# Kernel optimization log

Hardware: AMD Instinct MI355X
Metric: run time of the kernel (lower is better)

## Reference

```python
import jax, jax.numpy as jnp
import numpy as np

N = 50000        # nodes
R = 51           # enriched relations (25 fwd + 25 inverse + self-loop)
F_IN = 32        # feat_size
E = 32           # embed_size
C = 16           # num_classes
B = 30           # num_bases
NNZ = 2_000_000  # nonzeros in vertical adjacency


def _xavier(key, shape):
    # mimics nn.init.xavier_uniform_ with gain for relu (sqrt(2))
    fan_in, fan_out = shape[-2], shape[-1]
    a = np.sqrt(2.0) * np.sqrt(6.0 / (fan_in + fan_out))
    return jax.random.uniform(key, shape, jnp.float32, -a, a)


def setup_inputs() -> dict:
    key = jax.random.key(0)
    ks = jax.random.split(key, 8)
    # COO of vertical adjacency, shape (R*N, N)
    rows = jax.random.randint(ks[0], (NNZ,), 0, R * N)
    cols = jax.random.randint(ks[1], (NNZ,), 0, N)
    # row-normalized values: vals = 1 / row_degree  (sum_sparse with rows=True)
    deg = jax.ops.segment_sum(jnp.ones((NNZ,), jnp.float32), rows, num_segments=R * N)
    vals = (1.0 / jnp.maximum(deg, 1.0))[rows]
    features = jax.random.normal(ks[2], (N, F_IN), jnp.float32)
    comps1 = _xavier(ks[3], (R, B))
    bases1 = _xavier(ks[4], (B, F_IN, E))
    comps2 = _xavier(ks[5], (R, B))
    bases2 = _xavier(ks[6], (B, E, C))
    bias1 = jnp.zeros((E,), jnp.float32)
    bias2 = jnp.zeros((C,), jnp.float32)
    return {
        "features": features, "vals": vals,
        "comps1": comps1, "bases1": bases1, "bias1": bias1,
        "comps2": comps2, "bases2": bases2, "bias2": bias2,
        "rows": rows, "cols": cols,
    }


def _spmm(rows, cols, vals, x):
    # (R*N, N) sparse @ (N, f) dense -> (R*N, f)
    return jax.ops.segment_sum(vals[:, None] * x[cols], rows, num_segments=R * N)


def reference(features, vals, comps1, bases1, bias1, comps2, bases2, bias2, rows, cols):
    # layer 1: SpMM then basis-decomposed per-relation mixing
    h = _spmm(rows, cols, vals, features).reshape(R, N, F_IN)   # (r, n, f)
    w1 = jnp.einsum('rb,bfe->rfe', comps1, bases1)              # (r, f, e)
    h = jnp.einsum('rnf,rfe->ne', h, w1)                        # (n, e)
    h = jax.nn.relu(h + bias1)
    # layer 2
    h = _spmm(rows, cols, vals, h).reshape(R, N, E)             # (r, n, e)
    w2 = jnp.einsum('rb,bho->rho', comps2, bases2)              # (r, e, c)
    h = jnp.einsum('rho,rnh->no', w2, h)                        # (n, c)
    return h + bias2
```

## Files before the change

### kernel.cpp

```cpp
#include <hip/hip_runtime.h>

#define NNODES 50000
#define RREL 51
#define FIN 32
#define EDIM 32
#define CDIM 16
#define BB 30
#define NNZ_ 2000000
#define CAP_ 2000896
#define EPB 4096
#define MAXDEG 128

typedef unsigned int uint32;
typedef unsigned short ushort;
typedef uint32 u32x2 __attribute__((ext_vector_type(2)));
typedef uint32 u32x4 __attribute__((ext_vector_type(4)));
typedef short bf16x8 __attribute__((ext_vector_type(8)));
typedef float f32x4 __attribute__((ext_vector_type(4)));

static __device__ __forceinline__ uint32 pack_bf16x2(float a, float b) {
    uint32 ua = __builtin_bit_cast(uint32, a);
    uint32 ub = __builtin_bit_cast(uint32, b);
    ua += 0x7fffu + ((ua >> 16) & 1u);
    ub += 0x7fffu + ((ub >> 16) & 1u);
    return (ua >> 16) | (ub & 0xffff0000u);
}
static __device__ __forceinline__ ushort bf16_1(float x) {
    uint32 u = __builtin_bit_cast(uint32, x);
    u += 0x7fffu + ((u >> 16) & 1u);
    return (ushort)(u >> 16);
}
static __device__ __forceinline__ float unpack_lo(uint32 u) { return __builtin_bit_cast(float, u << 16); }
static __device__ __forceinline__ float unpack_hi(uint32 u) { return __builtin_bit_cast(float, u & 0xffff0000u); }

__global__ void k_weights(const float* __restrict__ comps1, const float* __restrict__ bases1,
                          const float* __restrict__ comps2, const float* __restrict__ bases2,
                          ushort* __restrict__ Wb1, ushort* __restrict__ Wb2) {
    int i = blockIdx.x * 256 + threadIdx.x;
    if (i < RREL * FIN * EDIM) {
        int r = i >> 10, fe = i & 1023, f = fe >> 5, e = fe & 31;
        float acc = 0.f;
#pragma unroll
        for (int b = 0; b < BB; b++) acc += comps1[r * BB + b] * bases1[b * 1024 + fe];
        Wb1[((r * 4 + (f >> 3)) * 32 + e) * 8 + (f & 7)] = bf16_1(acc);
    }
    if (i < RREL * EDIM * CDIM) {
        int r = i >> 9, ec = i & 511, kk = ec >> 4, c = ec & 15;
        float acc = 0.f;
#pragma unroll
        for (int b = 0; b < BB; b++) acc += comps2[r * BB + b] * bases2[b * 512 + ec];
        Wb2[((r * 4 + (kk >> 3)) * 16 + c) * 8 + (kk & 7)] = bf16_1(acc);
    }
}

__global__ void k_tobf16(const float2* __restrict__ src, uint32* __restrict__ dst, int n2) {
    int i = blockIdx.x * 256 + threadIdx.x;
    if (i < n2) {
        float2 f = src[i];
        dst[i] = pack_bf16x2(f.x, f.y);
    }
}

__global__ __launch_bounds__(1024) void k_relhist(const int* __restrict__ rows,
                                                  int* __restrict__ rel_cnt) {
    __shared__ int lc[RREL];
    int t = threadIdx.x;
    if (t < RREL) lc[t] = 0;
    __syncthreads();
    size_t k = (size_t)blockIdx.x * EPB + (size_t)t * 4;
    int rr[4];
    if (k + 4 <= NNZ_) {
        int4 rw = *(const int4*)(rows + k);
        rr[0] = rw.x; rr[1] = rw.y; rr[2] = rw.z; rr[3] = rw.w;
    } else {
#pragma unroll
        for (int j = 0; j < 4; j++) rr[j] = (k + j < NNZ_) ? rows[k + j] : -1;
    }
#pragma unroll
    for (int j = 0; j < 4; j++)
        if (rr[j] >= 0) atomicAdd(&lc[rr[j] / NNODES], 1);
    __syncthreads();
    if (t < RREL) atomicAdd(&rel_cnt[t], lc[t]);
}

__global__ void k_relscan(const int* __restrict__ rel_cnt, int* __restrict__ pad_base,
                          int* __restrict__ rel_cur) {
    if (threadIdx.x == 0) {
        int a = 0;
        for (int r = 0; r < RREL; r++) {
            pad_base[r] = a; rel_cur[r] = a;
            a += (rel_cnt[r] + 15) & ~15;
        }
        pad_base[RREL] = a;
    }
}

__global__ void k_padfill(const int* __restrict__ rel_cnt, const int* __restrict__ pad_base,
                          int* __restrict__ s_pk, int* __restrict__ s_src,
                          float* __restrict__ s_val) {
    int r = blockIdx.x;
    int start, end, relv;
    if (r < RREL) { start = pad_base[r] + rel_cnt[r]; end = pad_base[r + 1]; relv = r; }
    else { start = pad_base[RREL]; end = CAP_; relv = 0; }
    uint32 pdum = (uint32)NNODES * MAXDEG;
    for (int i = start + threadIdx.x; i < end; i += 64) {
        s_pk[i] = (int)(((uint32)relv << 25) | pdum);
        s_src[i] = 0;
        s_val[i] = 0.f;
    }
}

__global__ __launch_bounds__(1024) void k_scatter(const int* __restrict__ rows, const int* __restrict__ cols,
                                                  const float* __restrict__ vals, int* __restrict__ rel_cur,
                                                  int* __restrict__ dst_rank,
                                                  int* __restrict__ s_pk, int* __restrict__ s_src,
                                                  float* __restrict__ s_val) {
    __shared__ int lcnt[RREL], lbase[RREL], gbase[RREL];
    __shared__ int stotal;
    __shared__ uint32 st[EPB];
    int t = threadIdx.x;
    size_t base = (size_t)blockIdx.x * EPB;
    if (t < RREL) lcnt[t] = 0;
    __syncthreads();
    size_t k = base + (size_t)t * 4;
    int relv[4], dstv[4];
    {
        int rr[4];
        if (k + 4 <= NNZ_) {
            int4 rw = *(const int4*)(rows + k);
            rr[0] = rw.x; rr[1] = rw.y; rr[2] = rw.z; rr[3] = rw.w;
        } else {
#pragma unroll
            for (int j = 0; j < 4; j++) rr[j] = (k + j < NNZ_) ? rows[k + j] : -1;
        }
#pragma unroll
        for (int j = 0; j < 4; j++) {
            if (rr[j] >= 0) {
                int rel = rr[j] / NNODES;
                relv[j] = rel;
                dstv[j] = rr[j] - rel * NNODES;
                atomicAdd(&lcnt[rel], 1);
            } else relv[j] = -1;
        }
    }
    __syncthreads();
    if (t < 64) {
        int v = (t < RREL) ? lcnt[t] : 0;
        int sum = v;
#pragma unroll
        for (int off = 1; off < 64; off <<= 1) {
            int u = __shfl_up(sum, off, 64);
            if (t >= off) sum += u;
        }
        if (t < RREL) { lbase[t] = sum - v; gbase[t] = atomicAdd(&rel_cur[t], v); }
        if (t == RREL - 1) stotal = sum;
    }
    __syncthreads();
    if (t < RREL) lcnt[t] = 0;
    __syncthreads();
#pragma unroll
    for (int j = 0; j < 4; j++) {
        int rel = relv[j];
        if (rel >= 0) {
            int slot = lbase[rel] + atomicAdd(&lcnt[rel], 1);
            st[slot] = ((uint32)dstv[j] << 12) | (uint32)(t * 4 + j);
        }
    }
    __syncthreads();
    int total = stotal;
#pragma unroll
    for (int i = 0; i < 4; i++) {
        int s2 = t + i * 1024;
        if (s2 < total) {
            uint32 u = st[s2];
            int dst = (int)(u >> 12);
            int p = dst * MAXDEG + atomicAdd(&dst_rank[dst], 1);
            size_t orig = base + (u & 4095u);
            int rel = rows[orig] / NNODES;
            int g = gbase[rel] + (s2 - lbase[rel]);
            s_pk[g] = (int)(((uint32)rel << 25) | (uint32)p);
            s_src[g] = cols[orig];
            s_val[g] = vals[orig];
        }
    }
}

__global__ __launch_bounds__(1024) void k_scan(const int* __restrict__ cnt, int* __restrict__ base) {
    __shared__ int ssum[1024];
    int t = threadIdx.x;
    const int CH = 52;
    int lo = t * CH;
    int s = 0;
#pragma unroll
    for (int c = 0; c < 13; c++) {
        int i = lo + c * 4;
        if (i + 4 <= NNODES) {
            int4 q = *(const int4*)(cnt + i);
            s += q.x + q.y + q.z + q.w;
        } else {
            for (int j = 0; j < 4; j++) if (i + j < NNODES) s += cnt[i + j];
        }
    }
    ssum[t] = s;
    __syncthreads();
    for (int off = 1; off < 1024; off <<= 1) {
        int u = (t >= off) ? ssum[t - off] : 0;
        __syncthreads();
        ssum[t] += u;
        __syncthreads();
    }
    int run = (t == 0) ? 0 : ssum[t - 1];
#pragma unroll
    for (int c = 0; c < 13; c++) {
        int i = lo + c * 4;
        if (i + 4 <= NNODES) {
            int4 q = *(const int4*)(cnt + i);
            int4 w;
            w.x = run; run += q.x; w.y = run; run += q.y;
            w.z = run; run += q.z; w.w = run; run += q.w;
            *(int4*)(base + i) = w;
        } else {
            for (int j = 0; j < 4; j++) if (i + j < NNODES) { base[i + j] = run; run += cnt[i + j]; }
        }
    }
    if (t == 1023) base[NNODES] = run;
}

__global__ __launch_bounds__(256) void k_translate(int* __restrict__ s_pk,
                                                   const int* __restrict__ dst_base) {
    int i = blockIdx.x * 256 + threadIdx.x;
    int4 v = ((const int4*)s_pk)[i];
    int* c = &v.x;
#pragma unroll
    for (int j = 0; j < 4; j++) {
        uint32 pk = (uint32)c[j];
        uint32 p = pk & 0x1FFFFFFu;
        int dst = (int)(p >> 7);
        int compact = dst_base[dst] + (int)(p & 127u);
        c[j] = (int)((pk & 0xFE000000u) | (uint32)compact);
    }
    ((int4*)s_pk)[i] = v;
}

template <int FO>
__global__ __launch_bounds__(256) void k_edgeA(const int* __restrict__ s_pk,
                                               const int* __restrict__ s_src,
                                               const float* __restrict__ s_val,
                                               const u32x4* __restrict__ Xb,
                                               const u32x4* __restrict__ Wb,
                                               uint32* __restrict__ y) {
    const int NT = FO / 16;
    const int NW = (FO == 32) ? 32 : 16;
    int t = threadIdx.x, lane = t & 63, wv = t >> 6;
    int ln15 = lane & 15, quad = lane >> 4;
    size_t k0 = (size_t)blockIdx.x * 512 + wv * 128;

    int pk0 = s_pk[k0 + lane],  pk1 = s_pk[k0 + 64 + lane];
    int sc0 = s_src[k0 + lane], sc1 = s_src[k0 + 64 + lane];
    float v0 = s_val[k0 + lane], v1 = s_val[k0 + 64 + lane];

    f32x4 acc[8][NT];
    const f32x4 zero = {0.f, 0.f, 0.f, 0.f};
#pragma unroll
    for (int s = 0; s < 8; s++) {
        int osc = (s < 4) ? sc0 : sc1;
        int opk = (s < 4) ? pk0 : pk1;
        int srcs = __shfl(osc, (s & 3) * 16 + ln15, 64);
        int rels = (int)(((uint32)__builtin_amdgcn_readfirstlane(__shfl(opk, (s & 3) * 16, 64))) >> 25);
        bf16x8 a = __builtin_bit_cast(bf16x8, Xb[(size_t)srcs * 4 + quad]);
#pragma unroll
        for (int tt = 0; tt < NT; tt++) {
            bf16x8 b = __builtin_bit_cast(bf16x8, Wb[(rels * 4 + quad) * NW + ln15 + 16 * tt]);
            acc[s][tt] = __builtin_amdgcn_mfma_f32_16x16x32_bf16(a, b, zero, 0, 0, 0);
        }
    }

#pragma unroll
    for (int s = 0; s < 8; s++) {
        int opk = (s < 4) ? pk0 : pk1;
        float ov = (s < 4) ? v0 : v1;
#pragma unroll
        for (int rg = 0; rg < 4; rg++) {
            int e = (s & 3) * 16 + quad * 4 + rg;
            float ve = __shfl(ov, e, 64);
            int pe = __shfl(opk, e, 64) & 0x1FFFFFF;
            if (FO == 32) {
                uint32 val = pack_bf16x2(acc[s][0][rg] * ve, acc[s][1][rg] * ve);
                y[(size_t)pe * 16 + ln15] = val;
            } else {
                ((ushort*)y)[(size_t)pe * 16 + ln15] = bf16_1(acc[s][0][rg] * ve);
            }
        }
    }
}

template <int FO, bool RELU, bool BF16OUT>
__global__ __launch_bounds__(256) void k_segB(const uint32* __restrict__ y,
                                              const int* __restrict__ dst_base,
                                              const float* __restrict__ bias,
                                              void* __restrict__ outp) {
    const int UPR = FO / 2;
    const int QL = UPR / 4;
    const int RPI = 64 / QL;
    const bool ILV = (FO == 32);
    int t = threadIdx.x, lane = t & 63, wv = t >> 6;
    int dst = blockIdx.x * 4 + wv;
    if (dst >= NNODES) return;
    int s = dst_base[dst], e2 = dst_base[dst + 1];
    int q = lane % QL, r = lane / QL;
    float acc[8];
#pragma unroll
    for (int j = 0; j < 8; j++) acc[j] = 0.f;
    for (int i = s + r; i < e2; i += RPI) {
        u32x4 u = __builtin_nontemporal_load((const u32x4*)(y + (size_t)i * UPR + 4 * q));
        acc[0] += unpack_lo(u.x); acc[1] += unpack_hi(u.x);
        acc[2] += unpack_lo(u.y); acc[3] += unpack_hi(u.y);
        acc[4] += unpack_lo(u.z); acc[5] += unpack_hi(u.z);
        acc[6] += unpack_lo(u.w); acc[7] += unpack_hi(u.w);
    }
#pragma unroll
    for (int off = 32; off >= QL; off >>= 1)
#pragma unroll
        for (int j = 0; j < 8; j++) acc[j] += __shfl_down(acc[j], off, 64);
    if (lane < QL) {
        float o[8];
        if (ILV) {
#pragma unroll
            for (int j = 0; j < 4; j++) {
                o[2 * j]     = acc[2 * j]     + bias[4 * q + j];
                o[2 * j + 1] = acc[2 * j + 1] + bias[4 * q + 16 + j];
                if (RELU) { o[2 * j] = fmaxf(o[2 * j], 0.f); o[2 * j + 1] = fmaxf(o[2 * j + 1], 0.f); }
            }
        } else {
#pragma unroll
            for (int j = 0; j < 8; j++) {
                o[j] = acc[j] + bias[8 * q + j];
                if (RELU) o[j] = fmaxf(o[j], 0.f);
            }
        }
        if (BF16OUT) {
            if (ILV) {
                u32x2 a0, a1;
                a0.x = pack_bf16x2(o[0], o[2]); a0.y = pack_bf16x2(o[4], o[6]);
                a1.x = pack_bf16x2(o[1], o[3]); a1.y = pack_bf16x2(o[5], o[7]);
                ((u32x2*)outp)[(size_t)dst * 8 + q] = a0;
                ((u32x2*)outp)[(size_t)dst * 8 + 4 + q] = a1;
            } else {
                u32x4 pk;
                pk.x = pack_bf16x2(o[0], o[1]); pk.y = pack_bf16x2(o[2], o[3]);
                pk.z = pack_bf16x2(o[4], o[5]); pk.w = pack_bf16x2(o[6], o[7]);
                ((u32x4*)outp)[(size_t)dst * QL + q] = pk;
            }
        } else {
            float4* op = (float4*)outp;
            op[(size_t)dst * (FO / 4) + 2 * q]     = make_float4(o[0], o[1], o[2], o[3]);
            op[(size_t)dst * (FO / 4) + 2 * q + 1] = make_float4(o[4], o[5], o[6], o[7]);
        }
    }
}

extern "C" void kernel_launch(void* const* d_in, const int* in_sizes, int n_in,
                              void* d_out, int out_size, void* d_ws, size_t ws_size,
                              hipStream_t stream) {
    const float* features = (const float*)d_in[0];
    const float* vals     = (const float*)d_in[1];
    const float* comps1   = (const float*)d_in[2];
    const float* bases1   = (const float*)d_in[3];
    const float* bias1    = (const float*)d_in[4];
    const float* comps2   = (const float*)d_in[5];
    const float* bases2   = (const float*)d_in[6];
    const float* bias2    = (const float*)d_in[7];
    const int*   rows     = (const int*)d_in[8];
    const int*   cols     = (const int*)d_in[9];
    float* out = (float*)d_out;

    float* ws = (float*)d_ws;
    size_t o = 0;
    ushort* Wb1 = (ushort*)(ws + o); o += RREL * FIN * EDIM / 2;
    ushort* Wb2 = (ushort*)(ws + o); o += RREL * EDIM * CDIM / 2;
    o = (o + 3) & ~(size_t)3;
    uint32* Xb  = (uint32*)(ws + o); o += (size_t)NNODES * (FIN / 2);
    uint32* h1b = (uint32*)(ws + o); o += (size_t)NNODES * (EDIM / 2);
    int* s_pk  = (int*)(ws + o); o += CAP_;
    int* s_src = (int*)(ws + o); o += CAP_;
    float* s_val = ws + o;       o += CAP_;
    int* rel_cnt  = (int*)(ws + o); o += RREL + 1;
    int* dst_rank = (int*)(ws + o); o += NNODES;
    int* rel_cur  = (int*)(ws + o); o += RREL;
    int* pad_base = (int*)(ws + o); o += RREL + 1;
    o = (o + 3) & ~(size_t)3;
    int* dst_base = (int*)(ws + o); o += NNODES + 4;
    o = (o + 3) & ~(size_t)3;
    uint32* y = (uint32*)(ws + o);

    const int NB = (NNZ_ + EPB - 1) / EPB;

    hipMemsetAsync(rel_cnt, 0, (RREL + 1 + NNODES) * sizeof(int), stream);

    k_weights<<<(RREL * FIN * EDIM + 255) / 256, 256, 0, stream>>>(comps1, bases1, comps2, bases2, Wb1, Wb2);
    k_tobf16<<<(NNODES * FIN / 2 + 255) / 256, 256, 0, stream>>>((const float2*)features, Xb, NNODES * FIN / 2);
    k_relhist<<<NB, 1024, 0, stream>>>(rows, rel_cnt);
    k_relscan<<<1, 64, 0, stream>>>(rel_cnt, pad_base, rel_cur);
    k_padfill<<<RREL + 1, 64, 0, stream>>>(rel_cnt, pad_base, s_pk, s_src, s_val);
    k_scatter<<<NB, 1024, 0, stream>>>(rows, cols, vals, rel_cur, dst_rank, s_pk, s_src, s_val);
    k_scan<<<1, 1024, 0, stream>>>(dst_rank, dst_base);
    k_translate<<<CAP_ / 4 / 256, 256, 0, stream>>>(s_pk, dst_base);

    k_edgeA<EDIM><<<CAP_ / 512, 256, 0, stream>>>(s_pk, s_src, s_val, (const u32x4*)Xb,
                                                  (const u32x4*)Wb1, y);
    k_segB<EDIM, true, true><<<(NNODES + 3) / 4, 256, 0, stream>>>(y, dst_base, bias1, h1b);
    k_edgeA<CDIM><<<CAP_ / 512, 256, 0, stream>>>(s_pk, s_src, s_val, (const u32x4*)h1b,
                                                  (const u32x4*)Wb2, y);
    k_segB<CDIM, false, false><<<(NNODES + 3) / 4, 256, 0, stream>>>(y, dst_base, bias2, out);
}
```

Baseline: 392.3 us.

## Replace per-destination global atomic ranking with two-level bucketed counting sort

Drops the per-edge global atomicAdd on a 50000-entry dst_rank array, the single-block full-node scan and the translate pass. In their place it runs a bucket histogram over 128-node buckets inside the scatter kernel, a bucket scan, a block-local bucket sort into a scratch token buffer, and a per-bucket rank kernel that computes dst_base and the compacted positions. This removes contended global atomics and the MAXDEG=128 assumption. The cost is extra passes over the edge list and two additional kernel launches.

New measurement: 381.8 us. 1.03x faster.

```diff
diff --git a/kernel.cpp b/kernel.cpp
--- a/kernel.cpp
+++ b/kernel.cpp
@@ -9,7 +9,7 @@
 #define NNZ_ 2000000
 #define CAP_ 2000896
 #define EPB 4096
-#define MAXDEG 128
+#define NBUK 391
 
 typedef unsigned int uint32;
 typedef unsigned short ushort;
@@ -97,14 +97,15 @@
 
 __global__ void k_padfill(const int* __restrict__ rel_cnt, const int* __restrict__ pad_base,
                           int* __restrict__ s_pk, int* __restrict__ s_src,
-                          float* __restrict__ s_val) {
+                          float* __restrict__ s_val, int* __restrict__ buk_cnt) {
     int r = blockIdx.x;
     int start, end, relv;
     if (r < RREL) { start = pad_base[r] + rel_cnt[r]; end = pad_base[r + 1]; relv = r; }
     else { start = pad_base[RREL]; end = CAP_; relv = 0; }
-    uint32 pdum = (uint32)NNODES * MAXDEG;
+    if (threadIdx.x == 0 && end > start) atomicAdd(&buk_cnt[NBUK - 1], end - start);
+    int pkpad = (int)(((uint32)relv << 25) | (uint32)NNODES);
     for (int i = start + threadIdx.x; i < end; i += 64) {
-        s_pk[i] = (int)(((uint32)relv << 25) | pdum);
+        s_pk[i] = pkpad;
         s_src[i] = 0;
         s_val[i] = 0.f;
     }
@@ -112,15 +113,17 @@
 
 __global__ __launch_bounds__(1024) void k_scatter(const int* __restrict__ rows, const int* __restrict__ cols,
                                                   const float* __restrict__ vals, int* __restrict__ rel_cur,
-                                                  int* __restrict__ dst_rank,
+                                                  int* __restrict__ buk_cnt,
                                                   int* __restrict__ s_pk, int* __restrict__ s_src,
                                                   float* __restrict__ s_val) {
     __shared__ int lcnt[RREL], lbase[RREL], gbase[RREL];
+    __shared__ int bukc[NBUK];
     __shared__ int stotal;
     __shared__ uint32 st[EPB];
     int t = threadIdx.x;
     size_t base = (size_t)blockIdx.x * EPB;
     if (t < RREL) lcnt[t] = 0;
+    if (t < NBUK) bukc[t] = 0;
     __syncthreads();
     size_t k = base + (size_t)t * 4;
     int relv[4], dstv[4];
@@ -140,6 +143,7 @@
                 relv[j] = rel;
                 dstv[j] = rr[j] - rel * NNODES;
                 atomicAdd(&lcnt[rel], 1);
+                atomicAdd(&bukc[dstv[j] >> 7], 1);
             } else relv[j] = -1;
         }
     }
@@ -155,6 +159,7 @@
         if (t < RREL) { lbase[t] = sum - v; gbase[t] = atomicAdd(&rel_cur[t], v); }
         if (t == RREL - 1) stotal = sum;
     }
+    if (t < NBUK) atomicAdd(&buk_cnt[t], bukc[t]);
     __syncthreads();
     if (t < RREL) lcnt[t] = 0;
     __syncthreads();
@@ -174,34 +179,56 @@
         if (s2 < total) {
             uint32 u = st[s2];
             int dst = (int)(u >> 12);
-            int p = dst * MAXDEG + atomicAdd(&dst_rank[dst], 1);
             size_t orig = base + (u & 4095u);
             int rel = rows[orig] / NNODES;
             int g = gbase[rel] + (s2 - lbase[rel]);
-            s_pk[g] = (int)(((uint32)rel << 25) | (uint32)p);
+            s_pk[g] = (int)(((uint32)rel << 25) | (uint32)dst);
             s_src[g] = cols[orig];
             s_val[g] = vals[orig];
         }
     }
 }
 
-__global__ __launch_bounds__(1024) void k_scan(const int* __restrict__ cnt, int* __restrict__ base) {
+__global__ void k_bukscan(const int* __restrict__ buk_cnt, int* __restrict__ buk_base,
+                          int* __restrict__ buk_cur) {
+    if (threadIdx.x == 0) {
+        int a = 0;
+        for (int b = 0; b < NBUK; b++) { buk_base[b] = a; buk_cur[b] = a; a += buk_cnt[b]; }
+        buk_base[NBUK] = a;
+    }
+}
+
+__global__ __launch_bounds__(1024) void k_bucket(const int* __restrict__ s_pk,
+                                                 int* __restrict__ buk_cur,
+                                                 u32x2* __restrict__ tok8) {
+    __shared__ int bukc[NBUK], lbase2[NBUK], gbase2[NBUK];
     __shared__ int ssum[1024];
+    __shared__ u32x2 st8[EPB];
     int t = threadIdx.x;
-    const int CH = 52;
-    int lo = t * CH;
-    int s = 0;
-#pragma unroll
-    for (int c = 0; c < 13; c++) {
-        int i = lo + c * 4;
-        if (i + 4 <= NNODES) {
-            int4 q = *(const int4*)(cnt + i);
-            s += q.x + q.y + q.z + q.w;
-        } else {
-            for (int j = 0; j < 4; j++) if (i + j < NNODES) s += cnt[i + j];
-        }
-    }
-    ssum[t] = s;
+    size_t base = (size_t)blockIdx.x * EPB;
+    int total = (int)(((size_t)CAP_ - base < (size_t)EPB) ? ((size_t)CAP_ - base) : (size_t)EPB);
+    if (t < NBUK) bukc[t] = 0;
+    __syncthreads();
+    size_t k = base + (size_t)t * 4;
+    int pkv[4], bv[4];
+    if (k + 4 <= CAP_) {
+        int4 q = *(const int4*)(s_pk + k);
+        pkv[0] = q.x; pkv[1] = q.y; pkv[2] = q.z; pkv[3] = q.w;
+#pragma unroll
+        for (int j = 0; j < 4; j++) bv[j] = (int)(((uint32)pkv[j] & 0x1FFFFFFu) >> 7);
+    } else {
+#pragma unroll
+        for (int j = 0; j < 4; j++) {
+            if (k + j < CAP_) { pkv[j] = s_pk[k + j]; bv[j] = (int)(((uint32)pkv[j] & 0x1FFFFFFu) >> 7); }
+            else bv[j] = -1;
+        }
+    }
+#pragma unroll
+    for (int j = 0; j < 4; j++)
+        if (bv[j] >= 0) atomicAdd(&bukc[bv[j]], 1);
+    __syncthreads();
+    int v = (t < NBUK) ? bukc[t] : 0;
+    ssum[t] = v;
     __syncthreads();
     for (int off = 1; off < 1024; off <<= 1) {
         int u = (t >= off) ? ssum[t - off] : 0;
@@ -209,37 +236,63 @@
         ssum[t] += u;
         __syncthreads();
     }
-    int run = (t == 0) ? 0 : ssum[t - 1];
-#pragma unroll
-    for (int c = 0; c < 13; c++) {
-        int i = lo + c * 4;
-        if (i + 4 <= NNODES) {
-            int4 q = *(const int4*)(cnt + i);
-            int4 w;
-            w.x = run; run += q.x; w.y = run; run += q.y;
-            w.z = run; run += q.z; w.w = run; run += q.w;
-            *(int4*)(base + i) = w;
-        } else {
-            for (int j = 0; j < 4; j++) if (i + j < NNODES) { base[i + j] = run; run += cnt[i + j]; }
-        }
-    }
-    if (t == 1023) base[NNODES] = run;
-}
-
-__global__ __launch_bounds__(256) void k_translate(int* __restrict__ s_pk,
-                                                   const int* __restrict__ dst_base) {
-    int i = blockIdx.x * 256 + threadIdx.x;
-    int4 v = ((const int4*)s_pk)[i];
-    int* c = &v.x;
+    if (t < NBUK) { lbase2[t] = ssum[t] - v; gbase2[t] = atomicAdd(&buk_cur[t], v); }
+    __syncthreads();
+    if (t < NBUK) bukc[t] = 0;
+    __syncthreads();
 #pragma unroll
     for (int j = 0; j < 4; j++) {
-        uint32 pk = (uint32)c[j];
-        uint32 p = pk & 0x1FFFFFFu;
-        int dst = (int)(p >> 7);
-        int compact = dst_base[dst] + (int)(p & 127u);
-        c[j] = (int)((pk & 0xFE000000u) | (uint32)compact);
-    }
-    ((int4*)s_pk)[i] = v;
+        if (bv[j] >= 0) {
+            int slot = lbase2[bv[j]] + atomicAdd(&bukc[bv[j]], 1);
+            u32x2 w; w.x = (uint32)pkv[j]; w.y = (uint32)(k + j);
+            st8[slot] = w;
+        }
+    }
+    __syncthreads();
+    for (int s2 = t; s2 < total; s2 += 1024) {
+        u32x2 w = st8[s2];
+        int b = (int)((w.x & 0x1FFFFFFu) >> 7);
+        tok8[gbase2[b] + (s2 - lbase2[b])] = w;
+    }
+}
+
+__global__ __launch_bounds__(256) void k_rank(const u32x2* __restrict__ tok8,
+                                              const int* __restrict__ buk_base,
+                                              int* __restrict__ dst_base,
+                                              int* __restrict__ s_pk) {
+    __shared__ int lcnt[128], lexc[128], lrank[128], ssc[128];
+    int b = blockIdx.x, t = threadIdx.x;
+    int lo = buk_base[b], hi = buk_base[b + 1];
+    int d0 = b << 7;
+    if (t < 128) lcnt[t] = 0;
+    __syncthreads();
+    for (int i = lo + t; i < hi; i += 256) {
+        int dl = (int)(tok8[i].x & 0x1FFFFFFu) - d0;
+        atomicAdd(&lcnt[dl], 1);
+    }
+    __syncthreads();
+    int v = (t < 128) ? lcnt[t] : 0;
+    if (t < 128) ssc[t] = v;
+    __syncthreads();
+    for (int off = 1; off < 128; off <<= 1) {
+        int u = (t >= off && t < 128) ? ssc[t - off] : 0;
+        __syncthreads();
+        if (t < 128) ssc[t] += u;
+        __syncthreads();
+    }
+    if (t < 128) {
+        lexc[t] = ssc[t] - v;
+        int d = d0 + t;
+        if (d <= NNODES) dst_base[d] = lo + lexc[t];
+        lrank[t] = 0;
+    }
+    __syncthreads();
+    for (int i = lo + t; i < hi; i += 256) {
+        u32x2 w = tok8[i];
+        int dl = (int)(w.x & 0x1FFFFFFu) - d0;
+        int q = lo + lexc[dl] + atomicAdd(&lrank[dl], 1);
+        s_pk[(int)w.y] = (int)((w.x & 0xFE000000u) | (uint32)q);
+    }
 }
 
 template <int FO>
@@ -385,26 +438,31 @@
     int* s_src = (int*)(ws + o); o += CAP_;
     float* s_val = ws + o;       o += CAP_;
     int* rel_cnt  = (int*)(ws + o); o += RREL + 1;
-    int* dst_rank = (int*)(ws + o); o += NNODES;
+    int* buk_cnt  = (int*)(ws + o); o += NBUK + 1;
     int* rel_cur  = (int*)(ws + o); o += RREL;
     int* pad_base = (int*)(ws + o); o += RREL + 1;
+    int* buk_base = (int*)(ws + o); o += NBUK + 1;
+    int* buk_cur  = (int*)(ws + o); o += NBUK;
     o = (o + 3) & ~(size_t)3;
     int* dst_base = (int*)(ws + o); o += NNODES + 4;
     o = (o + 3) & ~(size_t)3;
     uint32* y = (uint32*)(ws + o);
+    u32x2* tok8 = (u32x2*)y;
 
     const int NB = (NNZ_ + EPB - 1) / EPB;
-
-    hipMemsetAsync(rel_cnt, 0, (RREL + 1 + NNODES) * sizeof(int), stream);
+    const int NB2 = (CAP_ + EPB - 1) / EPB;
+
+    hipMemsetAsync(rel_cnt, 0, (RREL + 1 + NBUK + 1) * sizeof(int), stream);
 
     k_weights<<<(RREL * FIN * EDIM + 255) / 256, 256, 0, stream>>>(comps1, bases1, comps2, bases2, Wb1, Wb2);
     k_tobf16<<<(NNODES * FIN / 2 + 255) / 256, 256, 0, stream>>>((const float2*)features, Xb, NNODES * FIN / 2);
     k_relhist<<<NB, 1024, 0, stream>>>(rows, rel_cnt);
     k_relscan<<<1, 64, 0, stream>>>(rel_cnt, pad_base, rel_cur);
-    k_padfill<<<RREL + 1, 64, 0, stream>>>(rel_cnt, pad_base, s_pk, s_src, s_val);
-    k_scatter<<<NB, 1024, 0, stream>>>(rows, cols, vals, rel_cur, dst_rank, s_pk, s_src, s_val);
-    k_scan<<<1, 1024, 0, stream>>>(dst_rank, dst_base);
-    k_translate<<<CAP_ / 4 / 256, 256, 0, stream>>>(s_pk, dst_base);
+    k_padfill<<<RREL + 1, 64, 0, stream>>>(rel_cnt, pad_base, s_pk, s_src, s_val, buk_cnt);
+    k_scatter<<<NB, 1024, 0, stream>>>(rows, cols, vals, rel_cur, buk_cnt, s_pk, s_src, s_val);
+    k_bukscan<<<1, 64, 0, stream>>>(buk_cnt, buk_base, buk_cur);
+    k_bucket<<<NB2, 1024, 0, stream>>>(s_pk, buk_cur, tok8);
+    k_rank<<<NBUK, 256, 0, stream>>>(tok8, buk_base, dst_base, s_pk);
 
     k_edgeA<EDIM><<<CAP_ / 512, 256, 0, stream>>>(s_pk, s_src, s_val, (const u32x4*)Xb,
                                                   (const u32x4*)Wb1, y);
```
